# Kernel tuning notes

Measured on AMD Instinct MI355X. Metric: run time of the kernel, lower is better.

Reference implementation:

```python
import jax, jax.numpy as jnp
import numpy as np

B, S, D, H = 2, 2048, 2048, 16
HD = D // H  # 128


def _rope_tables(seq_len, half_dim, theta=10000.0):
    freqs = 1.0 / (theta ** (np.arange(0, half_dim, dtype=np.float32) / half_dim))
    t = np.arange(seq_len, dtype=np.float32)
    ang = np.outer(t, freqs)  # [S, HD//2]
    return jnp.asarray(np.cos(ang)), jnp.asarray(np.sin(ang))


def setup_inputs() -> dict:
    key = jax.random.key(0)
    kx, kq, kk, kv, ko = jax.random.split(key, 5)
    cos, sin = _rope_tables(S, HD // 2)
    return {
        "x": jax.random.normal(kx, (B, S, D), dtype=jnp.float32),
        "cos": cos,  # [S, HD//2]
        "sin": sin,  # [S, HD//2]
        "wq": jax.random.normal(kq, (D, D), dtype=jnp.float32) * 0.02,
        "wk": jax.random.normal(kk, (D, D), dtype=jnp.float32) * 0.02,
        "wv": jax.random.normal(kv, (D, D), dtype=jnp.float32) * 0.02,
        "wo": jax.random.normal(ko, (D, D), dtype=jnp.float32) * 0.02,
    }


def _apply_rotary(t, cos, sin):
    # t: [B, S, H, HD]; rotate consecutive pairs (complex multiply)
    t2 = t.reshape(*t.shape[:-1], HD // 2, 2)
    te, to = t2[..., 0], t2[..., 1]
    c = cos[None, :, None, :]
    s = sin[None, :, None, :]
    out = jnp.stack([te * c - to * s, te * s + to * c], axis=-1)
    return out.reshape(t.shape)


def reference(x, cos, sin, wq, wk, wv, wo):
    xq = (x @ wq).reshape(B, S, H, HD)
    xk = (x @ wk).reshape(B, S, H, HD)
    xv = (x @ wv).reshape(B, S, H, HD)
    # FAITHFUL to source: rotary applied to xq and xv (NOT xk)
    xq = _apply_rotary(xq, cos, sin)
    xv = _apply_rotary(xv, cos, sin)
    q = xq.transpose(0, 2, 1, 3)  # [B,H,S,HD]
    k = xk.transpose(0, 2, 1, 3)
    v = xv.transpose(0, 2, 1, 3)
    scores = jnp.einsum("bhqd,bhkd->bhqk", q, k) / jnp.sqrt(jnp.float32(HD))
    mask = jnp.triu(jnp.full((S, S), -jnp.inf, dtype=scores.dtype), k=1)
    scores = scores + mask[None, None, :, :]
    probs = jax.nn.softmax(scores, axis=-1)
    out = jnp.einsum("bhqk,bhkd->bhqd", probs, v)  # [B,H,S,HD]
    out = out.transpose(0, 2, 1, 3).reshape(B, S, D)
    return out @ wo
```

## Files before the change

### kernel.cpp

```cpp
#include <hip/hip_runtime.h>
#include <hip/hip_bf16.h>

typedef short short8 __attribute__((ext_vector_type(8)));
typedef float f32x4 __attribute__((ext_vector_type(4)));
typedef int int4v __attribute__((ext_vector_type(4)));

#define B_ 2
#define S_ 2048
#define D_ 2048
#define H_ 16
#define HD_ 128
#define K_ 2048

#define GLL16(gp, lp) __builtin_amdgcn_global_load_lds( \
    (const __attribute__((address_space(1))) void*)(gp), \
    (__attribute__((address_space(3))) void*)(lp), 16, 0, 0)

__device__ inline ushort f2bf(float f) {
    union { float f; unsigned u; } v; v.f = f;
    unsigned r = v.u + 0x7FFFu + ((v.u >> 16) & 1u);
    return (ushort)(r >> 16);
}
__device__ inline float bf2f(ushort b) {
    union { unsigned u; float f; } v; v.u = ((unsigned)b) << 16;
    return v.f;
}

__global__ void cast_kernel(const float* __restrict__ src, ushort* __restrict__ dst, int n4) {
    int i = blockIdx.x * blockDim.x + threadIdx.x;
    if (i >= n4) return;
    float4 v = reinterpret_cast<const float4*>(src)[i];
    ushort4 o;
    o.x = f2bf(v.x); o.y = f2bf(v.y); o.z = f2bf(v.z); o.w = f2bf(v.w);
    reinterpret_cast<ushort4*>(dst)[i] = o;
}

__global__ __launch_bounds__(256) void cast_transpose_kernel(const float* __restrict__ src,
                                                             ushort* __restrict__ dst) {
    __shared__ ushort tile[64][72];
    const int bk = blockIdx.y * 64, bn = blockIdx.x * 64;
    const int t = threadIdx.x;
    #pragma unroll
    for (int it = 0; it < 4; ++it) {
        int id = t + it * 256;
        int row = id >> 4;
        int c4 = (id & 15) * 4;
        float4 v = *reinterpret_cast<const float4*>(&src[(size_t)(bk + row) * D_ + bn + c4]);
        ushort4 o; o.x = f2bf(v.x); o.y = f2bf(v.y); o.z = f2bf(v.z); o.w = f2bf(v.w);
        *reinterpret_cast<ushort4*>(&tile[row][c4]) = o;
    }
    __syncthreads();
    #pragma unroll
    for (int it = 0; it < 4; ++it) {
        int id = t + it * 256;
        int n = id >> 4;
        int c4 = (id & 15) * 4;
        ushort4 o;
        o.x = tile[c4 + 0][n]; o.y = tile[c4 + 1][n];
        o.z = tile[c4 + 2][n]; o.w = tile[c4 + 3][n];
        *reinterpret_cast<ushort4*>(&dst[(size_t)(bn + n) * D_ + bk + c4]) = o;
    }
}

__global__ void rope_kernel(ushort* __restrict__ t, const float* __restrict__ cosT,
                            const float* __restrict__ sinT, int npairs) {
    int pid = blockIdx.x * blockDim.x + threadIdx.x;
    if (pid >= npairs) return;
    int i = pid & 63;
    int s = (pid >> 6) & (S_ - 1);
    unsigned pr = reinterpret_cast<unsigned*>(t)[pid];
    float e = bf2f((ushort)(pr & 0xFFFFu));
    float o = bf2f((ushort)(pr >> 16));
    float c = cosT[s * 64 + i];
    float sn = sinT[s * 64 + i];
    float oe = e * c - o * sn;
    float oo = e * sn + o * c;
    unsigned outp = ((unsigned)f2bf(oo) << 16) | (unsigned)f2bf(oe);
    reinterpret_cast<unsigned*>(t)[pid] = outp;
}

#define BAR8() __builtin_amdgcn_s_barrier()
#define VMC0() asm volatile("s_waitcnt vmcnt(0)" ::: "memory")

template<int MODE>
__global__ __launch_bounds__(512, 2) void gemm8(const ushort* __restrict__ A,
        const ushort* __restrict__ Bt, ushort* __restrict__ q0, ushort* __restrict__ k0,
        ushort* __restrict__ v0, float* __restrict__ outf, int nbx) {
    constexpr int NC      = (MODE == 0) ? 4 : 2;
    constexpr int BN      = (MODE == 0) ? 256 : 128;
    constexpr int BHROWS  = BN / 2;
    constexpr int BHBYTES = BHROWS * 128;
    constexpr int BSTRIDE = 32768 + 2 * BHBYTES;
    constexpr int WROWS   = BHROWS / 2;

    extern __shared__ char smem[];
    const int tid = threadIdx.x, lane = tid & 63, wv = tid >> 6;
    const int wm = wv >> 2, wn = wv & 3;
    const int l15 = lane & 15, lg = lane >> 4;
    const int nwg = (int)gridDim.x, cpx = nwg >> 3;
    const int swzb = ((int)blockIdx.x & 7) * cpx + ((int)blockIdx.x >> 3);
    const int bn = (swzb % nbx) * BN, bm = (swzb / nbx) * 256;

    f32x4 acc[8][NC] = {};

    const int grl = wv * 8 + (lane >> 3);
    const int swc = (((lane & 7) ^ ((lane >> 3) & 7)) * 8);
    const ushort* Ag = A + (size_t)(bm + grl) * K_ + swc;
    const ushort* Bg = Bt + (size_t)(bn + grl) * K_ + swc;
    const size_t rowHA = (size_t)128 * K_;
    const size_t rowHB = (size_t)BHROWS * K_;
    const size_t row64 = (size_t)64 * K_;

#define VMC() do { if (MODE == 0) asm volatile("s_waitcnt vmcnt(2)" ::: "memory"); \
                   else           asm volatile("s_waitcnt vmcnt(1)" ::: "memory"); } while (0)
#define STAGE_A(t, h) do { if ((t) < 32) { \
        const ushort* g = Ag + (size_t)(h) * rowHA + (size_t)(t) * 64; \
        char* l = smem + (((t) & 1) ? BSTRIDE : 0) + ((h) << 14) + (wv << 10); \
        GLL16(g, l); GLL16(g + row64, l + 8192); } } while (0)
#define STAGE_B(t, h) do { if ((t) < 32) { \
        const ushort* g = Bg + (size_t)(h) * rowHB + (size_t)(t) * 64; \
        char* l = smem + (((t) & 1) ? BSTRIDE : 0) + 32768 + (h) * BHBYTES + (wv << 10); \
        GLL16(g, l); if (MODE == 0) GLL16(g + row64, l + 8192); } } while (0)

    const int colsw0 = (lg * 16) ^ ((l15 & 7) << 4);
    const int colsw1 = (64 + lg * 16) ^ ((l15 & 7) << 4);
    const char* abase0 = smem + (wm << 14);
    const char* bbase0 = smem + 32768 + (wn >> 1) * BHBYTES;
    const char* abase1 = abase0 + BSTRIDE;
    const char* bbase1 = bbase0 + BSTRIDE;
    const int brow = ((wn & 1) * WROWS + l15) * 128;

#define LDA(ab, q, cs) do { _Pragma("unroll") for (int f = 0; f < 4; ++f) \
        a[f] = *reinterpret_cast<const short8*>((ab) + ((q) * 64 + f * 16 + l15) * 128 + (cs)); } while (0)
#define LDB(bb, cs) do { _Pragma("unroll") for (int c = 0; c < NC; ++c) \
        b[c] = *reinterpret_cast<const short8*>((bb) + brow + c * 2048 + (cs)); } while (0)
#define MM(q) do { __builtin_amdgcn_s_setprio(1); \
        _Pragma("unroll") for (int f = 0; f < 4; ++f) \
        _Pragma("unroll") for (int c = 0; c < NC; ++c) \
            acc[(q) * 4 + f][c] = __builtin_amdgcn_mfma_f32_16x16x32_bf16(a[f], b[c], acc[(q) * 4 + f][c], 0, 0, 0); \
        __builtin_amdgcn_s_setprio(0); } while (0)

    STAGE_A(0, 0); STAGE_A(0, 1); STAGE_B(0, 0); STAGE_B(0, 1);
    STAGE_B(1, 0);
    VMC();
    BAR8();

    for (int i = 0; i < 16; ++i) {
        const int t1 = 2 * i + 1, s0 = 2 * i + 2, s1 = 2 * i + 3;
        short8 a[4], b[NC];
        LDB(bbase0, colsw0); LDA(abase0, 0, colsw0);
        STAGE_A(t1, 0);
        BAR8(); MM(0); BAR8();
        LDA(abase0, 1, colsw0);
        STAGE_A(t1, 1);
        BAR8(); MM(1); BAR8();
        LDB(bbase0, colsw1); LDA(abase0, 0, colsw1);
        STAGE_B(t1, 1);
        BAR8(); MM(0); BAR8();
        LDA(abase0, 1, colsw1);
        STAGE_B(s0, 0);
        if (s0 < 32) VMC(); else VMC0();
        BAR8(); MM(1); BAR8();
        LDB(bbase1, colsw0); LDA(abase1, 0, colsw0);
        STAGE_A(s0, 0);
        BAR8(); MM(0); BAR8();
        LDA(abase1, 1, colsw0);
        STAGE_A(s0, 1);
        BAR8(); MM(1); BAR8();
        LDB(bbase1, colsw1); LDA(abase1, 0, colsw1);
        STAGE_B(s0, 1);
        BAR8(); MM(0); BAR8();
        LDA(abase1, 1, colsw1);
        STAGE_B(s1, 0);
        if (s1 < 32) VMC(); else VMC0();
        BAR8(); MM(1); BAR8();
    }

    const int colbase = bn + wn * (BN / 4);
    if (MODE == 0) {
        const int seg = colbase >> 11;
        ushort* segp = (seg == 0) ? q0 : ((seg == 1) ? k0 : v0);
        #pragma unroll
        for (int rf = 0; rf < 8; ++rf)
            #pragma unroll
            for (int c = 0; c < NC; ++c)
                #pragma unroll
                for (int j = 0; j < 4; ++j) {
                    int row = bm + wm * 128 + rf * 16 + lg * 4 + j;
                    int col = colbase + c * 16 + l15;
                    int bb = row >> 11, s = row & (S_ - 1);
                    int h = (col >> 7) & (H_ - 1), d = col & (HD_ - 1);
                    segp[(((size_t)(bb * H_ + h)) * S_ + s) * HD_ + d] = f2bf(acc[rf][c][j]);
                }
    } else {
        #pragma unroll
        for (int rf = 0; rf < 8; ++rf)
            #pragma unroll
            for (int c = 0; c < NC; ++c)
                #pragma unroll
                for (int j = 0; j < 4; ++j) {
                    int row = bm + wm * 128 + rf * 16 + lg * 4 + j;
                    int col = colbase + c * 16 + l15;
                    outf[(size_t)row * D_ + col] = acc[rf][c][j];
                }
    }
#undef VMC
#undef STAGE_A
#undef STAGE_B
#undef LDA
#undef LDB
#undef MM
}

__global__ __launch_bounds__(256) void attn4(const ushort* __restrict__ Qm,
        const ushort* __restrict__ Km, const ushort* __restrict__ Vm,
        ushort* __restrict__ Om) {
    __shared__ __align__(16) ushort Kb[2][64 * 128];
    __shared__ __align__(16) ushort Vt[2][128][72];
    const int tid = threadIdx.x, lane = tid & 63, wv = tid >> 6;
    const int l15 = lane & 15, lg = lane >> 4;
    const int qt = 31 - (int)blockIdx.y;
    const int bh = blockIdx.x;
    const size_t base = (size_t)bh * S_ * HD_;
    const int qrow0 = qt * 64 + wv * 16;
    const float C = 0.1275174f;

    short8 qf[4];
    {
        const ushort* qp = Qm + base + (size_t)(qrow0 + l15) * HD_;
        #pragma unroll
        for (int c = 0; c < 4; ++c)
            qf[c] = *reinterpret_cast<const short8*>(qp + c * 32 + lg * 8);
    }
    f32x4 oacc[8] = {};
    float mS = -1e30f, lS = 0.f;
    const int ntiles = qt + 1;
    const int qv = wv * 16 + l15;

    {
        #pragma unroll
        for (int c = 0; c < 4; ++c) {
            int row = wv * 16 + c * 4 + (lane >> 4);
            GLL16(Km + base + (size_t)row * HD_ + (((lane & 15) ^ (row & 7)) << 3),
                  &Kb[0][wv * 2048 + c * 512]);
        }
        const ushort* vp = Vm + base + (size_t)lane * HD_ + wv * 32;
        #pragma unroll
        for (int cc = 0; cc < 4; ++cc) {
            int4v v = *reinterpret_cast<const int4v*>(vp + cc * 8);
            const ushort* e = reinterpret_cast<const ushort*>(&v);
            #pragma unroll
            for (int j = 0; j < 8; ++j) Vt[0][wv * 32 + cc * 8 + j][lane] = e[j];
        }
    }
    __syncthreads();

    int cur = 0;
    for (int kt = 0; kt < ntiles; ++kt) {
        const bool pfn = (kt + 1 < ntiles);
        int4v vr[4];
        if (pfn) {
            const int r0 = (kt + 1) * 64;
            #pragma unroll
            for (int c = 0; c < 4; ++c) {
                int row = wv * 16 + c * 4 + (lane >> 4);
                GLL16(Km + base + (size_t)(r0 + row) * HD_ + (((lane & 15) ^ (row & 7)) << 3),
                      &Kb[cur ^ 1][wv * 2048 + c * 512]);
            }
            const ushort* vp = Vm + base + (size_t)(r0 + lane) * HD_ + wv * 32;
            #pragma unroll
            for (int cc = 0; cc < 4; ++cc)
                vr[cc] = *reinterpret_cast<const int4v*>(vp + cc * 8);
        }
        f32x4 sacc[4] = {};
        const ushort* Kc = &Kb[cur][0];
        __builtin_amdgcn_s_setprio(1);
        #pragma unroll
        for (int ct = 0; ct < 4; ++ct) {
            const int row = ct * 16 + l15;
            const int sw = (row & 7) << 3;
            #pragma unroll
            for (int c = 0; c < 4; ++c) {
                short8 kf = *reinterpret_cast<const short8*>(
                    Kc + row * 128 + ((c * 32 + lg * 8) ^ sw));
                sacc[ct] = __builtin_amdgcn_mfma_f32_16x16x32_bf16(kf, qf[c], sacc[ct], 0, 0, 0);
            }
        }
        __builtin_amdgcn_s_setprio(0);

        float t16[16];
        #pragma unroll
        for (int ct = 0; ct < 4; ++ct)
            #pragma unroll
            for (int j = 0; j < 4; ++j) t16[ct * 4 + j] = sacc[ct][j];
        if (kt == qt) {
            #pragma unroll
            for (int ct = 0; ct < 4; ++ct)
                #pragma unroll
                for (int j = 0; j < 4; ++j)
                    if (ct * 16 + lg * 4 + j > qv) t16[ct * 4 + j] = -1e30f;
        }
        float mx[8];
        #pragma unroll
        for (int i = 0; i < 8; ++i) mx[i] = fmaxf(t16[i], t16[i + 8]);
        #pragma unroll
        for (int i = 0; i < 4; ++i) mx[i] = fmaxf(mx[i], mx[i + 4]);
        float m64 = fmaxf(fmaxf(mx[0], mx[1]), fmaxf(mx[2], mx[3]));
        m64 = fmaxf(m64, __shfl_xor(m64, 16));
        m64 = fmaxf(m64, __shfl_xor(m64, 32));
        if (!__all(m64 - mS <= 47.0f)) {
            float mnew = fmaxf(mS, m64);
            float corr = __builtin_amdgcn_exp2f((mS - mnew) * C);
            lS *= corr;
            #pragma unroll
            for (int dt = 0; dt < 8; ++dt)
                #pragma unroll
                for (int j = 0; j < 4; ++j) oacc[dt][j] *= corr;
            mS = mnew;
        }
        const float mcc = mS * C;
        float p[16];
        #pragma unroll
        for (int i = 0; i < 16; ++i)
            p[i] = __builtin_amdgcn_exp2f(fmaf(t16[i], C, -mcc));
        float sm[8];
        #pragma unroll
        for (int i = 0; i < 8; ++i) sm[i] = p[i] + p[i + 8];
        #pragma unroll
        for (int i = 0; i < 4; ++i) sm[i] = sm[i] + sm[i + 4];
        float psum = (sm[0] + sm[1]) + (sm[2] + sm[3]);
        psum += __shfl_xor(psum, 16);
        psum += __shfl_xor(psum, 32);
        lS += psum;

        unsigned dw[8];
        #pragma unroll
        for (int ct = 0; ct < 4; ++ct)
            #pragma unroll
            for (int u = 0; u < 2; ++u) {
                __hip_bfloat162 h2 = __float22bfloat162_rn(
                    float2{p[ct * 4 + 2 * u], p[ct * 4 + 2 * u + 1]});
                dw[ct * 2 + u] = *reinterpret_cast<unsigned*>(&h2);
            }
        #pragma unroll
        for (int c2 = 0; c2 < 2; ++c2) {
            int4v pfd;
            #pragma unroll
            for (int d = 0; d < 4; ++d) {
                int srcl = (lg & 1) * 32 + (d >> 1) * 16 + l15;
                int r0 = __shfl((int)dw[(2 * c2) * 2 + (d & 1)], srcl);
                int r1 = __shfl((int)dw[(2 * c2 + 1) * 2 + (d & 1)], srcl);
                pfd[d] = (lg & 2) ? r1 : r0;
            }
            short8 pf = *reinterpret_cast<short8*>(&pfd);
            __builtin_amdgcn_s_setprio(1);
            #pragma unroll
            for (int dt = 0; dt < 8; ++dt) {
                short8 vf = *reinterpret_cast<const short8*>(
                    &Vt[cur][dt * 16 + l15][c2 * 32 + lg * 8]);
                oacc[dt] = __builtin_amdgcn_mfma_f32_16x16x32_bf16(vf, pf, oacc[dt], 0, 0, 0);
            }
            __builtin_amdgcn_s_setprio(0);
        }
        if (pfn) {
            #pragma unroll
            for (int cc = 0; cc < 4; ++cc) {
                const ushort* e = reinterpret_cast<const ushort*>(&vr[cc]);
                #pragma unroll
                for (int j = 0; j < 8; ++j) Vt[cur ^ 1][wv * 32 + cc * 8 + j][lane] = e[j];
            }
        }
        __syncthreads();
        cur ^= 1;
    }
    const int b = bh >> 4, h = bh & (H_ - 1);
    const int q = qt * 64 + wv * 16 + l15;
    const float inv = 1.0f / lS;
    ushort* op = Om + ((size_t)(b * S_ + q)) * D_ + h * HD_;
    #pragma unroll
    for (int dt = 0; dt < 8; ++dt) {
        ushort4 o;
        o.x = f2bf(oacc[dt][0] * inv);
        o.y = f2bf(oacc[dt][1] * inv);
        o.z = f2bf(oacc[dt][2] * inv);
        o.w = f2bf(oacc[dt][3] * inv);
        *reinterpret_cast<ushort4*>(op + dt * 16 + lg * 4) = o;
    }
}

extern "C" void kernel_launch(void* const* d_in, const int* in_sizes, int n_in,
                              void* d_out, int out_size, void* d_ws, size_t ws_size,
                              hipStream_t stream) {
    const float* x    = (const float*)d_in[0];
    const float* cosT = (const float*)d_in[1];
    const float* sinT = (const float*)d_in[2];
    const float* wq   = (const float*)d_in[3];
    const float* wk   = (const float*)d_in[4];
    const float* wv   = (const float*)d_in[5];
    const float* wo   = (const float*)d_in[6];
    float* out = (float*)d_out;

    char* ws = (char*)d_ws;
    const size_t szX = (size_t)B_ * S_ * D_ * 2;
    const size_t szW = (size_t)D_ * D_ * 2;
    ushort* xb   = (ushort*)(ws);
    ushort* wcat = (ushort*)(ws + szX);
    ushort* woT  = (ushort*)(ws + szX + 3 * szW);
    ushort* q0   = (ushort*)(ws + szX + 4 * szW);
    ushort* k0   = (ushort*)(ws + szX + 4 * szW + szX);
    ushort* v0   = (ushort*)(ws + szX + 4 * szW + 2 * szX);
    ushort* att  = xb;

    hipFuncSetAttribute(reinterpret_cast<const void*>(&gemm8<0>),
                        hipFuncAttributeMaxDynamicSharedMemorySize, 131072);
    hipFuncSetAttribute(reinterpret_cast<const void*>(&gemm8<1>),
                        hipFuncAttributeMaxDynamicSharedMemorySize, 98304);

    const int nx = B_ * S_ * D_;
    cast_kernel<<<nx / 4 / 256, 256, 0, stream>>>(x, xb, nx / 4);
    dim3 tg(D_ / 64, D_ / 64);
    cast_transpose_kernel<<<tg, 256, 0, stream>>>(wq, wcat);
    cast_transpose_kernel<<<tg, 256, 0, stream>>>(wk, wcat + (size_t)D_ * D_);
    cast_transpose_kernel<<<tg, 256, 0, stream>>>(wv, wcat + 2 * (size_t)D_ * D_);
    cast_transpose_kernel<<<tg, 256, 0, stream>>>(wo, woT);

    gemm8<0><<<384, 512, 131072, stream>>>(xb, wcat, q0, k0, v0, nullptr, 24);

    const int npairs = B_ * S_ * H_ * 64;
    rope_kernel<<<npairs / 256, 256, 0, stream>>>(q0, cosT, sinT, npairs);
    rope_kernel<<<npairs / 256, 256, 0, stream>>>(v0, cosT, sinT, npairs);

    attn4<<<dim3(B_ * H_, S_ / 64), 256, 0, stream>>>(q0, k0, v0, att);

    gemm8<1><<<256, 512, 98304, stream>>>(att, woT, nullptr, nullptr, nullptr, out, 16);
}
```

Before: 277.7 us.

## Fuse RoPE into QKV GEMM epilogue, batch weight casts, use 128-row attention tiles

Rotary embedding for Q and V now runs inside the QKV GEMM epilogue, using a lane shuffle to fetch each pair partner. This removes two standalone RoPE kernels and their extra read/write passes. The four weight cast-transpose launches are merged into one launch indexed by blockIdx.z. Attention moves to 512-thread blocks covering 128 query rows with interleaved tile ordering and per-wave causal masking, which halves K/V reloads per query and changes load balance, at the cost of more register and occupancy pressure.

```diff
diff --git a/kernel.cpp b/kernel.cpp
--- a/kernel.cpp
+++ b/kernel.cpp
@@ -35,9 +35,15 @@
     reinterpret_cast<ushort4*>(dst)[i] = o;
 }
 
-__global__ __launch_bounds__(256) void cast_transpose_kernel(const float* __restrict__ src,
-                                                             ushort* __restrict__ dst) {
+__global__ __launch_bounds__(256) void cast_transpose4(
+        const float* __restrict__ s0, const float* __restrict__ s1,
+        const float* __restrict__ s2, const float* __restrict__ s3,
+        ushort* __restrict__ d0, ushort* __restrict__ d1,
+        ushort* __restrict__ d2, ushort* __restrict__ d3) {
     __shared__ ushort tile[64][72];
+    const int z = blockIdx.z;
+    const float* src = (z == 0) ? s0 : (z == 1) ? s1 : (z == 2) ? s2 : s3;
+    ushort* dst = (z == 0) ? d0 : (z == 1) ? d1 : (z == 2) ? d2 : d3;
     const int bk = blockIdx.y * 64, bn = blockIdx.x * 64;
     const int t = threadIdx.x;
     #pragma unroll
@@ -62,30 +68,14 @@
     }
 }
 
-__global__ void rope_kernel(ushort* __restrict__ t, const float* __restrict__ cosT,
-                            const float* __restrict__ sinT, int npairs) {
-    int pid = blockIdx.x * blockDim.x + threadIdx.x;
-    if (pid >= npairs) return;
-    int i = pid & 63;
-    int s = (pid >> 6) & (S_ - 1);
-    unsigned pr = reinterpret_cast<unsigned*>(t)[pid];
-    float e = bf2f((ushort)(pr & 0xFFFFu));
-    float o = bf2f((ushort)(pr >> 16));
-    float c = cosT[s * 64 + i];
-    float sn = sinT[s * 64 + i];
-    float oe = e * c - o * sn;
-    float oo = e * sn + o * c;
-    unsigned outp = ((unsigned)f2bf(oo) << 16) | (unsigned)f2bf(oe);
-    reinterpret_cast<unsigned*>(t)[pid] = outp;
-}
-
 #define BAR8() __builtin_amdgcn_s_barrier()
 #define VMC0() asm volatile("s_waitcnt vmcnt(0)" ::: "memory")
 
 template<int MODE>
 __global__ __launch_bounds__(512, 2) void gemm8(const ushort* __restrict__ A,
         const ushort* __restrict__ Bt, ushort* __restrict__ q0, ushort* __restrict__ k0,
-        ushort* __restrict__ v0, float* __restrict__ outf, int nbx) {
+        ushort* __restrict__ v0, float* __restrict__ outf,
+        const float* __restrict__ cosT, const float* __restrict__ sinT, int nbx) {
     constexpr int NC      = (MODE == 0) ? 4 : 2;
     constexpr int BN      = (MODE == 0) ? 256 : 128;
     constexpr int BHROWS  = BN / 2;
@@ -180,18 +170,32 @@
     if (MODE == 0) {
         const int seg = colbase >> 11;
         ushort* segp = (seg == 0) ? q0 : ((seg == 1) ? k0 : v0);
+        const bool dorope = (seg != 1);
+        const int dbase = colbase & 127;
         #pragma unroll
         for (int rf = 0; rf < 8; ++rf)
             #pragma unroll
-            for (int c = 0; c < NC; ++c)
+            for (int c = 0; c < NC; ++c) {
+                const int d = dbase + c * 16 + l15;
+                const int ih = d >> 1;
                 #pragma unroll
                 for (int j = 0; j < 4; ++j) {
                     int row = bm + wm * 128 + rf * 16 + lg * 4 + j;
                     int col = colbase + c * 16 + l15;
                     int bb = row >> 11, s = row & (S_ - 1);
-                    int h = (col >> 7) & (H_ - 1), d = col & (HD_ - 1);
-                    segp[(((size_t)(bb * H_ + h)) * S_ + s) * HD_ + d] = f2bf(acc[rf][c][j]);
+                    int h = (col >> 7) & (H_ - 1);
+                    float v = acc[rf][c][j];
+                    float outv;
+                    if (dorope) {
+                        float vp = __shfl_xor(v, 1);
+                        float cs = cosT[s * 64 + ih], sn = sinT[s * 64 + ih];
+                        outv = (l15 & 1) ? fmaf(vp, sn, v * cs) : fmaf(v, cs, -(vp * sn));
+                    } else {
+                        outv = v;
+                    }
+                    segp[(((size_t)(bb * H_ + h)) * S_ + s) * HD_ + d] = f2bf(outv);
                 }
+            }
     } else {
         #pragma unroll
         for (int rf = 0; rf < 8; ++rf)
@@ -212,17 +216,18 @@
 #undef MM
 }
 
-__global__ __launch_bounds__(256) void attn4(const ushort* __restrict__ Qm,
+__global__ __launch_bounds__(512, 4) void attn5(const ushort* __restrict__ Qm,
         const ushort* __restrict__ Km, const ushort* __restrict__ Vm,
         ushort* __restrict__ Om) {
     __shared__ __align__(16) ushort Kb[2][64 * 128];
     __shared__ __align__(16) ushort Vt[2][128][72];
     const int tid = threadIdx.x, lane = tid & 63, wv = tid >> 6;
     const int l15 = lane & 15, lg = lane >> 4;
-    const int qt = 31 - (int)blockIdx.y;
+    const int yy = (int)blockIdx.y;
+    const int qt = (yy < 8) ? (15 - 2 * yy) : (2 * (yy - 8));
     const int bh = blockIdx.x;
     const size_t base = (size_t)bh * S_ * HD_;
-    const int qrow0 = qt * 64 + wv * 16;
+    const int qrow0 = qt * 128 + wv * 16;
     const float C = 0.1275174f;
 
     short8 qf[4];
@@ -234,23 +239,23 @@
     }
     f32x4 oacc[8] = {};
     float mS = -1e30f, lS = 0.f;
-    const int ntiles = qt + 1;
-    const int qv = wv * 16 + l15;
+    const int ntiles = 2 * qt + 2;
+    const int kmask0 = 2 * qt + (wv >> 2);
 
     {
         #pragma unroll
-        for (int c = 0; c < 4; ++c) {
-            int row = wv * 16 + c * 4 + (lane >> 4);
+        for (int c = 0; c < 2; ++c) {
+            int row = wv * 8 + c * 4 + (lane >> 4);
             GLL16(Km + base + (size_t)row * HD_ + (((lane & 15) ^ (row & 7)) << 3),
-                  &Kb[0][wv * 2048 + c * 512]);
-        }
-        const ushort* vp = Vm + base + (size_t)lane * HD_ + wv * 32;
-        #pragma unroll
-        for (int cc = 0; cc < 4; ++cc) {
+                  &Kb[0][wv * 1024 + c * 512]);
+        }
+        const ushort* vp = Vm + base + (size_t)lane * HD_ + wv * 16;
+        #pragma unroll
+        for (int cc = 0; cc < 2; ++cc) {
             int4v v = *reinterpret_cast<const int4v*>(vp + cc * 8);
             const ushort* e = reinterpret_cast<const ushort*>(&v);
             #pragma unroll
-            for (int j = 0; j < 8; ++j) Vt[0][wv * 32 + cc * 8 + j][lane] = e[j];
+            for (int j = 0; j < 8; ++j) Vt[0][wv * 16 + cc * 8 + j][lane] = e[j];
         }
     }
     __syncthreads();
@@ -258,18 +263,18 @@
     int cur = 0;
     for (int kt = 0; kt < ntiles; ++kt) {
         const bool pfn = (kt + 1 < ntiles);
-        int4v vr[4];
+        int4v vr[2];
         if (pfn) {
             const int r0 = (kt + 1) * 64;
             #pragma unroll
-            for (int c = 0; c < 4; ++c) {
-                int row = wv * 16 + c * 4 + (lane >> 4);
+            for (int c = 0; c < 2; ++c) {
+                int row = wv * 8 + c * 4 + (lane >> 4);
                 GLL16(Km + base + (size_t)(r0 + row) * HD_ + (((lane & 15) ^ (row & 7)) << 3),
-                      &Kb[cur ^ 1][wv * 2048 + c * 512]);
-            }
-            const ushort* vp = Vm + base + (size_t)(r0 + lane) * HD_ + wv * 32;
-            #pragma unroll
-            for (int cc = 0; cc < 4; ++cc)
+                      &Kb[cur ^ 1][wv * 1024 + c * 512]);
+            }
+            const ushort* vp = Vm + base + (size_t)(r0 + lane) * HD_ + wv * 16;
+            #pragma unroll
+            for (int cc = 0; cc < 2; ++cc)
                 vr[cc] = *reinterpret_cast<const int4v*>(vp + cc * 8);
         }
         f32x4 sacc[4] = {};
@@ -293,12 +298,13 @@
         for (int ct = 0; ct < 4; ++ct)
             #pragma unroll
             for (int j = 0; j < 4; ++j) t16[ct * 4 + j] = sacc[ct][j];
-        if (kt == qt) {
+        if (kt >= kmask0) {
+            const int thr = qrow0 + l15 - kt * 64;
             #pragma unroll
             for (int ct = 0; ct < 4; ++ct)
                 #pragma unroll
                 for (int j = 0; j < 4; ++j)
-                    if (ct * 16 + lg * 4 + j > qv) t16[ct * 4 + j] = -1e30f;
+                    if (ct * 16 + lg * 4 + j > thr) t16[ct * 4 + j] = -1e30f;
         }
         float mx[8];
         #pragma unroll
@@ -364,17 +370,17 @@
         }
         if (pfn) {
             #pragma unroll
-            for (int cc = 0; cc < 4; ++cc) {
+            for (int cc = 0; cc < 2; ++cc) {
                 const ushort* e = reinterpret_cast<const ushort*>(&vr[cc]);
                 #pragma unroll
-                for (int j = 0; j < 8; ++j) Vt[cur ^ 1][wv * 32 + cc * 8 + j][lane] = e[j];
+                for (int j = 0; j < 8; ++j) Vt[cur ^ 1][wv * 16 + cc * 8 + j][lane] = e[j];
             }
         }
         __syncthreads();
         cur ^= 1;
     }
     const int b = bh >> 4, h = bh & (H_ - 1);
-    const int q = qt * 64 + wv * 16 + l15;
+    const int q = qrow0 + l15;
     const float inv = 1.0f / lS;
     ushort* op = Om + ((size_t)(b * S_ + q)) * D_ + h * HD_;
     #pragma unroll
@@ -418,19 +424,13 @@
 
     const int nx = B_ * S_ * D_;
     cast_kernel<<<nx / 4 / 256, 256, 0, stream>>>(x, xb, nx / 4);
-    dim3 tg(D_ / 64, D_ / 64);
-    cast_transpose_kernel<<<tg, 256, 0, stream>>>(wq, wcat);
-    cast_transpose_kernel<<<tg, 256, 0, stream>>>(wk, wcat + (size_t)D_ * D_);
-    cast_transpose_kernel<<<tg, 256, 0, stream>>>(wv, wcat + 2 * (size_t)D_ * D_);
-    cast_transpose_kernel<<<tg, 256, 0, stream>>>(wo, woT);
-
-    gemm8<0><<<384, 512, 131072, stream>>>(xb, wcat, q0, k0, v0, nullptr, 24);
-
-    const int npairs = B_ * S_ * H_ * 64;
-    rope_kernel<<<npairs / 256, 256, 0, stream>>>(q0, cosT, sinT, npairs);
-    rope_kernel<<<npairs / 256, 256, 0, stream>>>(v0, cosT, sinT, npairs);
-
-    attn4<<<dim3(B_ * H_, S_ / 64), 256, 0, stream>>>(q0, k0, v0, att);
-
-    gemm8<1><<<256, 512, 98304, stream>>>(att, woT, nullptr, nullptr, nullptr, out, 16);
-}
+    cast_transpose4<<<dim3(D_ / 64, D_ / 64, 4), 256, 0, stream>>>(
+        wq, wk, wv, wo, wcat, wcat + (size_t)D_ * D_, wcat + 2 * (size_t)D_ * D_, woT);
+
+    gemm8<0><<<384, 512, 131072, stream>>>(xb, wcat, q0, k0, v0, nullptr, cosT, sinT, 24);
+
+    attn5<<<dim3(B_ * H_, S_ / 128), 512, 0, stream>>>(q0, k0, v0, att);
+
+    gemm8<1><<<256, 512, 98304, stream>>>(att, woT, nullptr, nullptr, nullptr, out,
+                                          nullptr, nullptr, 16);
+}
```

Measured after the change: 292.8 us. 1.05x slower.
